# Performance work log

Measured on AMD Instinct MI355X. Metric: run time of the kernel, lower is better.

## Reference

```python
import jax, jax.numpy as jnp
import numpy as np

N_BITS = 8
Q_LEVELS = N_BITS ** 2 - 1  # note: original uses n_bits**2 - 1, not 2**n_bits - 1
GRID_RES = (128, 512, 2048)  # 2**7, 2**9, 2**11
BITWIDTH = 6
CODE_SIZE = 4


def _qround(x, axis):
    mn = jnp.min(x, axis=axis, keepdims=True)
    mx = jnp.max(x, axis=axis, keepdims=True)
    scale = jnp.maximum(mx - mn, 1e-8) / Q_LEVELS
    return jnp.round((x - mn) / scale) * scale + mn


def _ste(q, x):
    # straight-through estimator: forward q, gradient of x
    return jax.lax.stop_gradient(q - x) + x


def _qalinear(x, w, b):
    w_q = _ste(_qround(w, (-2, -1)), w)
    b_q = _ste(_qround(b, -1), b)
    return x @ w_q + b_q


def _grid(coords, indices, codebook, res):
    # coords: [N] in [-1, 1]; indices: [res, 2**bitwidth]; codebook: [2**bitwidth, code_size]
    soft_grid = jax.nn.softmax(indices, axis=-1) @ codebook           # [res, C]
    max_grid = codebook[jnp.argmax(indices, axis=1)]                  # [res, C]
    grid = _ste(max_grid, soft_grid)
    c = (coords + 1.0) / 2.0 * (res - 1)
    left = jnp.minimum(jnp.floor(c), res - 2).astype(jnp.int32)
    right = jnp.maximum(jnp.ceil(c), 1).astype(jnp.int32)
    w = (c - left)[..., None]                                         # [N, 1]
    return (1.0 - w) * grid[left] + w * grid[right]                   # [N, C]


def setup_inputs() -> dict:
    key = jax.random.key(0)
    ks = jax.random.split(key, 20)
    N = 1 << 20
    x_coord = jax.random.uniform(ks[0], (N, 1), jnp.float32, -1.0, 1.0)
    x_feat = jax.random.uniform(ks[1], (N, 1), jnp.float32, -1.0, 1.0)
    x = jnp.concatenate([x_feat, x_coord], axis=-1)  # last dim is the grid coordinate
    inp = {"x": x}
    for gi, res in enumerate(GRID_RES):
        inp[f"cb{gi}"] = 0.01 * jax.random.normal(ks[2 + 2 * gi], (2 ** BITWIDTH, CODE_SIZE), jnp.float32)
        inp[f"ind{gi}"] = 0.01 * jax.random.normal(ks[3 + 2 * gi], (res, 2 ** BITWIDTH), jnp.float32)
    dims = [(5, 64), (64, 64), (64, 64), (64, 64), (64, 1)]
    for li, (di, do) in enumerate(dims):
        inp[f"w{li}"] = (2 * jax.random.uniform(ks[8 + 2 * li], (di, do), jnp.float32) - 1) / np.sqrt(di)
        inp[f"b{li}"] = (2 * jax.random.uniform(ks[9 + 2 * li], (do,), jnp.float32) - 1) / np.sqrt(di)
    return inp


def reference(x, cb0, ind0, cb1, ind1, cb2, ind2,
              w0, b0, w1, b1, w2, b2, w3, b3, w4, b4):
    coords = x[..., -1]
    g = (_grid(coords, ind0, cb0, GRID_RES[0])
         + _grid(coords, ind1, cb1, GRID_RES[1])
         + _grid(coords, ind2, cb2, GRID_RES[2]))           # [N, 4]
    h = jnp.concatenate([g, x[..., :-1]], axis=-1)          # [N, 5]
    h = _qalinear(h, w0, b0)
    for w, b in ((w1, b1), (w2, b2), (w3, b3)):
        h = _qalinear(jax.nn.gelu(h, approximate=False), w, b)
    h = _qalinear(jax.nn.gelu(h, approximate=False), w4, b4)
    return jnp.tanh(h)
```

## Files before the change

kernel.cpp:

```cpp
#include <hip/hip_runtime.h>
#include <hip/hip_bf16.h>
#include <math.h>

#define WQ0 0
#define BQ0 320
#define WQ1 384
#define BQ1 4480
#define WQ2 4544
#define BQ2 8640
#define WQ3 8704
#define BQ3 12800
#define WQ4 12864
#define BQ4 12928
#define GT0 12932
#define GT1 13444
#define GT2 15492
#define FRAG_OFF 23684
#define NFRAG 28
#define W4P 38020
#define WSCALE 64.0f
#define WINV   0.015625f

typedef _Float16 f16x8 __attribute__((ext_vector_type(8)));
typedef _Float16 f16x2 __attribute__((ext_vector_type(2)));
typedef float floatx4 __attribute__((ext_vector_type(4)));
typedef float floatx2 __attribute__((ext_vector_type(2)));
typedef unsigned int uintx4 __attribute__((ext_vector_type(4)));

__device__ inline floatx4 mfma16(f16x8 a, f16x8 b, floatx4 c) {
    return __builtin_amdgcn_mfma_f32_16x16x32_f16(a, b, c, 0, 0, 0);
}
__device__ inline floatx2 splat2(float c) { return (floatx2){c, c}; }

__device__ inline unsigned int pkrtz(float a, float b) {
    auto r = __builtin_amdgcn_cvt_pkrtz(a, b);
    return __builtin_bit_cast(unsigned int, r);
}
__device__ inline unsigned int pack_f16(float a, float b) {
    unsigned short ua = __builtin_bit_cast(unsigned short, (_Float16)a);
    unsigned short ub = __builtin_bit_cast(unsigned short, (_Float16)b);
    return (unsigned int)ua | ((unsigned int)ub << 16);
}
__device__ inline f16x8 frag_from(uint2 a, uint2 b) {
    uintx4 u = {a.x, a.y, b.x, b.y};
    return __builtin_bit_cast(f16x8, u);
}
__device__ inline f16x2 h2(unsigned int u) { return __builtin_bit_cast(f16x2, u); }

#if __has_builtin(__builtin_amdgcn_fdot2)
__device__ inline float fdot2f(f16x2 a, f16x2 b, float c) {
    return __builtin_amdgcn_fdot2(a, b, c, false);
}
#else
__device__ inline float fdot2f(f16x2 a, f16x2 b, float c) {
    return fmaf((float)a[0], (float)b[0], fmaf((float)a[1], (float)b[1], c));
}
#endif

__device__ inline floatx2 gelu2(floatx2 x) {
    floatx2 ax = __builtin_elementwise_abs(x);
    floatx2 z  = ax * splat2(0.70710678118654752f);
    floatx2 den = __builtin_elementwise_fma(z, splat2(0.47047f), splat2(1.0f));
    floatx2 t;
    t.x = __builtin_amdgcn_rcpf(den.x);
    t.y = __builtin_amdgcn_rcpf(den.y);
    floatx2 p = __builtin_elementwise_fma(t, splat2(0.7478556f), splat2(-0.0958798f));
    p = __builtin_elementwise_fma(t, p, splat2(0.3480242f));
    p = p * t;
    floatx2 ea = (z * z) * splat2(-1.44269504088896f);
    floatx2 e;
    e.x = __builtin_amdgcn_exp2f(ea.x);
    e.y = __builtin_amdgcn_exp2f(ea.y);
    floatx2 er = __builtin_elementwise_fma(-p, e, splat2(1.0f));
    return __builtin_elementwise_fma(ax, er, x) * splat2(0.5f);
}

__device__ inline float tanh_fast(float x) {
    float e = __builtin_amdgcn_exp2f(x * 2.88539008177793f);
    return fmaf(-2.0f, __builtin_amdgcn_rcpf(e + 1.0f), 1.0f);
}

__device__ void block_minmax(float mn, float mx, float* omn, float* omx,
                             float* smn, float* smx) {
    __syncthreads();
    #pragma unroll
    for (int off = 32; off > 0; off >>= 1) {
        mn = fminf(mn, __shfl_down(mn, off));
        mx = fmaxf(mx, __shfl_down(mx, off));
    }
    int wid = threadIdx.x >> 6, lane = threadIdx.x & 63;
    if (lane == 0) { smn[wid] = mn; smx[wid] = mx; }
    __syncthreads();
    if (threadIdx.x == 0) {
        float a = smn[0], b = smx[0];
        for (int i = 1; i < 4; ++i) { a = fminf(a, smn[i]); b = fmaxf(b, smx[i]); }
        smn[0] = a; smx[0] = b;
    }
    __syncthreads();
    *omn = smn[0]; *omx = smx[0];
}

__device__ void quantize_tensor(const float* __restrict__ src, int n,
                                float* __restrict__ dst, float* smn, float* smx) {
    float mn = 3.4e38f, mx = -3.4e38f;
    for (int i = threadIdx.x; i < n; i += blockDim.x) {
        float v = src[i];
        mn = fminf(mn, v); mx = fmaxf(mx, v);
    }
    float gmn, gmx;
    block_minmax(mn, mx, &gmn, &gmx, smn, smx);
    float scale = fmaxf(gmx - gmn, 1e-8f) / 63.0f;
    for (int i = threadIdx.x; i < n; i += blockDim.x) {
        float v = src[i];
        dst[i] = rintf((v - gmn) / scale) * scale + gmn;
    }
}

__global__ void vinr_prep(
    const float* __restrict__ cb0, const float* __restrict__ ind0,
    const float* __restrict__ cb1, const float* __restrict__ ind1,
    const float* __restrict__ cb2, const float* __restrict__ ind2,
    const float* __restrict__ w0, const float* __restrict__ b0,
    const float* __restrict__ w1, const float* __restrict__ b1,
    const float* __restrict__ w2, const float* __restrict__ b2,
    const float* __restrict__ w3, const float* __restrict__ b3,
    const float* __restrict__ w4, const float* __restrict__ b4,
    float* __restrict__ ws)
{
    __shared__ float smn[4], smx[4];
    if (blockIdx.x < 10) {
        switch (blockIdx.x) {
            case 0: quantize_tensor(w0, 320, ws + WQ0, smn, smx); break;
            case 1: quantize_tensor(b0, 64, ws + BQ0, smn, smx); break;
            case 2: quantize_tensor(w1, 4096, ws + WQ1, smn, smx); break;
            case 3: quantize_tensor(b1, 64, ws + BQ1, smn, smx); break;
            case 4: quantize_tensor(w2, 4096, ws + WQ2, smn, smx); break;
            case 5: quantize_tensor(b2, 64, ws + BQ2, smn, smx); break;
            case 6: quantize_tensor(w3, 4096, ws + WQ3, smn, smx); break;
            case 7: quantize_tensor(b3, 64, ws + BQ3, smn, smx); break;
            case 8: quantize_tensor(w4, 64, ws + WQ4, smn, smx); break;
            case 9: quantize_tensor(b4, 1, ws + BQ4, smn, smx); break;
        }
    } else if (blockIdx.x < 21) {
        int r = (int)(blockIdx.x - 10) * 256 + (int)threadIdx.x;
        const float* ind = nullptr; const float* cb = nullptr; float* dst = nullptr;
        if (r < 128)       { ind = ind0 + r * 64;          cb = cb0; dst = ws + GT0 + r * 4; }
        else if (r < 640)  { int rr = r - 128;  ind = ind1 + rr * 64; cb = cb1; dst = ws + GT1 + rr * 4; }
        else if (r < 2688) { int rr = r - 640;  ind = ind2 + rr * 64; cb = cb2; dst = ws + GT2 + rr * 4; }
        if (dst) {
            float best = -3.4e38f; int bi = 0;
            for (int j = 0; j < 64; ++j) {
                float v = ind[j];
                if (v > best) { best = v; bi = j; }
            }
            #pragma unroll
            for (int d = 0; d < 4; ++d) dst[d] = cb[bi * 4 + d];
        }
    } else if (blockIdx.x < 45) {
        if (threadIdx.x < 64) {
            int fi = (int)blockIdx.x - 21;
            int lane = (int)threadIdx.x;
            int l = fi >> 3, s = (fi >> 2) & 1, ft = fi & 3;
            const float* w = (l == 0) ? w1 : (l == 1) ? w2 : w3;
            float mn = 3.4e38f, mx = -3.4e38f;
            for (int i = lane; i < 4096; i += 64) {
                float v = w[i];
                mn = fminf(mn, v); mx = fmaxf(mx, v);
            }
            #pragma unroll
            for (int off = 32; off > 0; off >>= 1) {
                mn = fminf(mn, __shfl_xor(mn, off));
                mx = fmaxf(mx, __shfl_xor(mx, off));
            }
            float scale = fmaxf(mx - mn, 1e-8f) / 63.0f;
            int q = lane >> 4, m15 = lane & 15;
            int n = ft * 16 + m15;
            f16x8 hi;
            #pragma unroll
            for (int j = 0; j < 8; ++j) {
                int k = s * 32 + q * 8 + j;
                float v = w[k * 64 + n];
                v = (rintf((v - mn) / scale) * scale + mn) * WSCALE;
                hi[j] = (_Float16)v;
            }
            f16x8* base = (f16x8*)(ws + FRAG_OFF);
            base[fi * 64 + lane] = hi;
        }
    } else if (blockIdx.x == 45) {
        int wv = (int)threadIdx.x >> 6;
        int lane = (int)threadIdx.x & 63;
        if (wv < 4) {
            float mn = 3.4e38f, mx = -3.4e38f;
            for (int i = lane; i < 320; i += 64) {
                float v = w0[i];
                mn = fminf(mn, v); mx = fmaxf(mx, v);
            }
            #pragma unroll
            for (int off = 32; off > 0; off >>= 1) {
                mn = fminf(mn, __shfl_xor(mn, off));
                mx = fmaxf(mx, __shfl_xor(mx, off));
            }
            float scale = fmaxf(mx - mn, 1e-8f) / 63.0f;
            int q = lane >> 4, m15 = lane & 15;
            int n = wv * 16 + m15;
            f16x8 hi;
            #pragma unroll
            for (int j = 0; j < 8; ++j) {
                int k = q * 8 + j;
                float v = 0.0f;
                if (k < 5) {
                    float vv = w0[k * 64 + n];
                    v = (rintf((vv - mn) / scale) * scale + mn) * WSCALE;
                }
                hi[j] = (_Float16)v;
            }
            f16x8* base = (f16x8*)(ws + FRAG_OFF);
            base[(24 + wv) * 64 + lane] = hi;
        }
    } else {
        if (threadIdx.x < 64) {
            int lane = (int)threadIdx.x;
            float v = w4[lane];
            float mn = v, mx = v;
            #pragma unroll
            for (int off = 32; off > 0; off >>= 1) {
                mn = fminf(mn, __shfl_xor(mn, off));
                mx = fmaxf(mx, __shfl_xor(mx, off));
            }
            float scale = fmaxf(mx - mn, 1e-8f) / 63.0f;
            if (lane < 32) {
                float q0 = (rintf((w4[2 * lane] - mn) / scale) * scale + mn) * WSCALE;
                float q1 = (rintf((w4[2 * lane + 1] - mn) / scale) * scale + mn) * WSCALE;
                unsigned int* wsU = (unsigned int*)ws;
                wsU[W4P + lane] = pack_f16(q0, q1);
            }
        }
    }
}

#define PSTR 38

__global__ __launch_bounds__(256, 4) void vinr_main(
    const float* __restrict__ x, const float* __restrict__ ws,
    float* __restrict__ out, int N)
{
    __shared__ __align__(16) unsigned int hlds[4 * 32 * PSTR];
    int wave = threadIdx.x >> 6, lane = threadIdx.x & 63;
    int q = lane >> 4, m15 = lane & 15;
    int p = lane & 31, half = lane >> 5;
    unsigned int* slice = hlds + wave * (32 * PSTR);

    int idx = (int)blockIdx.x * 128 + wave * 32 + p;
    int idxc = min(idx, N - 1);
    float2 xr = ((const float2*)x)[idxc];
    float feat  = xr.x;
    float coord = xr.y;

    float g0 = 0.f, g1 = 0.f, g2 = 0.f, g3 = 0.f;
    const int RES[3]  = {128, 512, 2048};
    const int GOFF[3] = {GT0, GT1, GT2};
    #pragma unroll
    for (int gi = 0; gi < 3; ++gi) {
        int res = RES[gi];
        float c = (coord + 1.0f) * 0.5f * (float)(res - 1);
        int left  = min((int)floorf(c), res - 2);
        int right = max((int)ceilf(c), 1);
        float w = c - (float)left;
        const float4* gt = (const float4*)(ws + GOFF[gi]);
        float4 gl = gt[left];
        float4 gr = gt[right];
        float wm = 1.0f - w;
        g0 += wm * gl.x + w * gr.x;
        g1 += wm * gl.y + w * gr.y;
        g2 += wm * gl.z + w * gr.z;
        g3 += wm * gl.w + w * gr.w;
    }

    const f16x8* fh = (const f16x8*)(ws + FRAG_OFF);
    f16x8 zfrag = __builtin_bit_cast(f16x8, (uintx4){0u, 0u, 0u, 0u});

    if (half == 0) {
        unsigned int* row = slice + p * PSTR;
        *(uint2*)row       = make_uint2(pack_f16(g0, g1), pack_f16(g2, g3));
        *(uint2*)(row + 2) = make_uint2(pack_f16(feat, 0.0f), 0u);
    }

    {
        f16x8 Wh[4];
        #pragma unroll
        for (int ft = 0; ft < 4; ++ft)
            Wh[ft] = fh[(24 + ft) * 64 + lane];
        f16x8 B[2];
        #pragma unroll
        for (int pt = 0; pt < 2; ++pt) {
            B[pt] = zfrag;
            if (q == 0) {
                const unsigned int* rp = slice + (pt * 16 + m15) * PSTR;
                B[pt] = frag_from(*(const uint2*)rp, *(const uint2*)(rp + 2));
            }
        }
        floatx4 acc[4][2];
        #pragma unroll
        for (int ft = 0; ft < 4; ++ft)
            #pragma unroll
            for (int pt = 0; pt < 2; ++pt)
                acc[ft][pt] = (floatx4){0.f, 0.f, 0.f, 0.f};
        #pragma unroll
        for (int ft = 0; ft < 4; ++ft)
            #pragma unroll
            for (int pt = 0; pt < 2; ++pt)
                acc[ft][pt] = mfma16(Wh[ft], B[pt], acc[ft][pt]);
        #pragma unroll
        for (int ft = 0; ft < 4; ++ft) {
            float4 b4 = *(const float4*)(ws + BQ0 + ft * 16 + q * 4);
            #pragma unroll
            for (int pt = 0; pt < 2; ++pt) {
                floatx4 av = acc[ft][pt];
                floatx2 a01 = __builtin_elementwise_fma((floatx2){av[0], av[1]},
                                  splat2(WINV), (floatx2){b4.x, b4.y});
                floatx2 a23 = __builtin_elementwise_fma((floatx2){av[2], av[3]},
                                  splat2(WINV), (floatx2){b4.z, b4.w});
                floatx2 v01 = gelu2(a01);
                floatx2 v23 = gelu2(a23);
                *(uint2*)(slice + (pt * 16 + m15) * PSTR + 8 * ft + 2 * q) =
                    make_uint2(pkrtz(v01.x, v01.y), pkrtz(v23.x, v23.y));
            }
        }
    }

    const int BQL[3] = {BQ1, BQ2, BQ3};
    #pragma unroll
    for (int l = 0; l < 3; ++l) {
        floatx4 acc[4][2];
        #pragma unroll
        for (int ft = 0; ft < 4; ++ft)
            #pragma unroll
            for (int pt = 0; pt < 2; ++pt)
                acc[ft][pt] = (floatx4){0.f, 0.f, 0.f, 0.f};

        #pragma unroll
        for (int s = 0; s < 2; ++s) {
            f16x8 Wh[4];
            #pragma unroll
            for (int ft = 0; ft < 4; ++ft)
                Wh[ft] = fh[((l * 2 + s) * 4 + ft) * 64 + lane];
            f16x8 B[2];
            #pragma unroll
            for (int pt = 0; pt < 2; ++pt) {
                const unsigned int* rp =
                    slice + (pt * 16 + m15) * PSTR + 16 * s + 4 * q;
                B[pt] = frag_from(*(const uint2*)rp, *(const uint2*)(rp + 2));
            }
            #pragma unroll
            for (int ft = 0; ft < 4; ++ft)
                #pragma unroll
                for (int pt = 0; pt < 2; ++pt)
                    acc[ft][pt] = mfma16(Wh[ft], B[pt], acc[ft][pt]);
        }
        #pragma unroll
        for (int ft = 0; ft < 4; ++ft) {
            float4 b4 = *(const float4*)(ws + BQL[l] + ft * 16 + q * 4);
            #pragma unroll
            for (int pt = 0; pt < 2; ++pt) {
                floatx4 av = acc[ft][pt];
                floatx2 a01 = __builtin_elementwise_fma((floatx2){av[0], av[1]},
                                  splat2(WINV), (floatx2){b4.x, b4.y});
                floatx2 a23 = __builtin_elementwise_fma((floatx2){av[2], av[3]},
                                  splat2(WINV), (floatx2){b4.z, b4.w});
                floatx2 v01 = gelu2(a01);
                floatx2 v23 = gelu2(a23);
                *(uint2*)(slice + (pt * 16 + m15) * PSTR + 8 * ft + 2 * q) =
                    make_uint2(pkrtz(v01.x, v01.y), pkrtz(v23.x, v23.y));
            }
        }
    }

    {
        const unsigned int* wsU = (const unsigned int*)ws;
        const unsigned int* base = slice + p * PSTR + 16 * half;
        int wb = W4P + 16 * half;
        float ah = 0.0f;
        #pragma unroll
        for (int c = 0; c < 8; ++c) {
            uint2 r = *(const uint2*)(base + 2 * c);
            ah = fdot2f(h2(r.x), h2(wsU[wb + 2 * c]),     ah);
            ah = fdot2f(h2(r.y), h2(wsU[wb + 2 * c + 1]), ah);
        }
        float acc4 = fmaf(ah, WINV, (half == 0) ? ws[BQ4] : 0.0f);
        acc4 += __shfl_xor(acc4, 32);
        if (half == 0 && idx < N) out[idx] = tanh_fast(acc4);
    }
}

extern "C" void kernel_launch(void* const* d_in, const int* in_sizes, int n_in,
                              void* d_out, int out_size, void* d_ws, size_t ws_size,
                              hipStream_t stream) {
    const float* x    = (const float*)d_in[0];
    const float* cb0  = (const float*)d_in[1];
    const float* ind0 = (const float*)d_in[2];
    const float* cb1  = (const float*)d_in[3];
    const float* ind1 = (const float*)d_in[4];
    const float* cb2  = (const float*)d_in[5];
    const float* ind2 = (const float*)d_in[6];
    const float* w0 = (const float*)d_in[7],  * b0 = (const float*)d_in[8];
    const float* w1 = (const float*)d_in[9],  * b1 = (const float*)d_in[10];
    const float* w2 = (const float*)d_in[11], * b2 = (const float*)d_in[12];
    const float* w3 = (const float*)d_in[13], * b3 = (const float*)d_in[14];
    const float* w4 = (const float*)d_in[15], * b4 = (const float*)d_in[16];
    float* ws  = (float*)d_ws;
    float* out = (float*)d_out;

    int N = in_sizes[0] / 2;

    vinr_prep<<<47, 256, 0, stream>>>(cb0, ind0, cb1, ind1, cb2, ind2,
                                      w0, b0, w1, b1, w2, b2, w3, b3, w4, b4, ws);
    int blocks = (N + 127) / 128;
    vinr_main<<<blocks, 256, 0, stream>>>(x, ws, out, N);
}
```

Baseline: 214.4 us.

## Keep MLP activations in registers by permuting weight fragment K-order

```diff
diff --git a/kernel.cpp b/kernel.cpp
--- a/kernel.cpp
+++ b/kernel.cpp
@@ -2,21 +2,15 @@
 #include <hip/hip_bf16.h>
 #include <math.h>
 
-#define WQ0 0
 #define BQ0 320
-#define WQ1 384
 #define BQ1 4480
-#define WQ2 4544
 #define BQ2 8640
-#define WQ3 8704
 #define BQ3 12800
-#define WQ4 12864
 #define BQ4 12928
 #define GT0 12932
 #define GT1 13444
 #define GT2 15492
 #define FRAG_OFF 23684
-#define NFRAG 28
 #define W4P 38020
 #define WSCALE 64.0f
 #define WINV   0.015625f
@@ -128,21 +122,16 @@
     float* __restrict__ ws)
 {
     __shared__ float smn[4], smx[4];
-    if (blockIdx.x < 10) {
+    if (blockIdx.x < 5) {
         switch (blockIdx.x) {
-            case 0: quantize_tensor(w0, 320, ws + WQ0, smn, smx); break;
-            case 1: quantize_tensor(b0, 64, ws + BQ0, smn, smx); break;
-            case 2: quantize_tensor(w1, 4096, ws + WQ1, smn, smx); break;
-            case 3: quantize_tensor(b1, 64, ws + BQ1, smn, smx); break;
-            case 4: quantize_tensor(w2, 4096, ws + WQ2, smn, smx); break;
-            case 5: quantize_tensor(b2, 64, ws + BQ2, smn, smx); break;
-            case 6: quantize_tensor(w3, 4096, ws + WQ3, smn, smx); break;
-            case 7: quantize_tensor(b3, 64, ws + BQ3, smn, smx); break;
-            case 8: quantize_tensor(w4, 64, ws + WQ4, smn, smx); break;
-            case 9: quantize_tensor(b4, 1, ws + BQ4, smn, smx); break;
-        }
-    } else if (blockIdx.x < 21) {
-        int r = (int)(blockIdx.x - 10) * 256 + (int)threadIdx.x;
+            case 0: quantize_tensor(b0, 64, ws + BQ0, smn, smx); break;
+            case 1: quantize_tensor(b1, 64, ws + BQ1, smn, smx); break;
+            case 2: quantize_tensor(b2, 64, ws + BQ2, smn, smx); break;
+            case 3: quantize_tensor(b3, 64, ws + BQ3, smn, smx); break;
+            case 4: quantize_tensor(b4, 1,  ws + BQ4, smn, smx); break;
+        }
+    } else if (blockIdx.x < 16) {
+        int r = (int)(blockIdx.x - 5) * 256 + (int)threadIdx.x;
         const float* ind = nullptr; const float* cb = nullptr; float* dst = nullptr;
         if (r < 128)       { ind = ind0 + r * 64;          cb = cb0; dst = ws + GT0 + r * 4; }
         else if (r < 640)  { int rr = r - 128;  ind = ind1 + rr * 64; cb = cb1; dst = ws + GT1 + rr * 4; }
@@ -156,9 +145,9 @@
             #pragma unroll
             for (int d = 0; d < 4; ++d) dst[d] = cb[bi * 4 + d];
         }
-    } else if (blockIdx.x < 45) {
+    } else if (blockIdx.x < 40) {
         if (threadIdx.x < 64) {
-            int fi = (int)blockIdx.x - 21;
+            int fi = (int)blockIdx.x - 16;
             int lane = (int)threadIdx.x;
             int l = fi >> 3, s = (fi >> 2) & 1, ft = fi & 3;
             const float* w = (l == 0) ? w1 : (l == 1) ? w2 : w3;
@@ -178,7 +167,7 @@
             f16x8 hi;
             #pragma unroll
             for (int j = 0; j < 8; ++j) {
-                int k = s * 32 + q * 8 + j;
+                int k = s * 32 + (j >> 2) * 16 + q * 4 + (j & 3);
                 float v = w[k * 64 + n];
                 v = (rintf((v - mn) / scale) * scale + mn) * WSCALE;
                 hi[j] = (_Float16)v;
@@ -186,7 +175,7 @@
             f16x8* base = (f16x8*)(ws + FRAG_OFF);
             base[fi * 64 + lane] = hi;
         }
-    } else if (blockIdx.x == 45) {
+    } else if (blockIdx.x == 40) {
         int wv = (int)threadIdx.x >> 6;
         int lane = (int)threadIdx.x & 63;
         if (wv < 4) {
@@ -229,28 +218,31 @@
             }
             float scale = fmaxf(mx - mn, 1e-8f) / 63.0f;
             if (lane < 32) {
-                float q0 = (rintf((w4[2 * lane] - mn) / scale) * scale + mn) * WSCALE;
-                float q1 = (rintf((w4[2 * lane + 1] - mn) / scale) * scale + mn) * WSCALE;
+                int t0 = 2 * lane, t1 = t0 + 1;
+                int f0 = ((t0 >> 5) * 32) + (((t0 >> 2) & 1) * 16)
+                       + (((t0 >> 3) & 3) * 4) + (t0 & 3);
+                int f1 = ((t1 >> 5) * 32) + (((t1 >> 2) & 1) * 16)
+                       + (((t1 >> 3) & 3) * 4) + (t1 & 3);
+                float q0 = (rintf((w4[f0] - mn) / scale) * scale + mn) * WSCALE;
+                float q1 = (rintf((w4[f1] - mn) / scale) * scale + mn) * WSCALE;
                 unsigned int* wsU = (unsigned int*)ws;
                 wsU[W4P + lane] = pack_f16(q0, q1);
             }
         }
     }
 }
-
-#define PSTR 38
 
 __global__ __launch_bounds__(256, 4) void vinr_main(
     const float* __restrict__ x, const float* __restrict__ ws,
     float* __restrict__ out, int N)
 {
-    __shared__ __align__(16) unsigned int hlds[4 * 32 * PSTR];
+    __shared__ __align__(16) uint4 ilds[4][32];
     int wave = threadIdx.x >> 6, lane = threadIdx.x & 63;
     int q = lane >> 4, m15 = lane & 15;
     int p = lane & 31, half = lane >> 5;
-    unsigned int* slice = hlds + wave * (32 * PSTR);
-
-    int idx = (int)blockIdx.x * 128 + wave * 32 + p;
+
+    int base = (int)blockIdx.x * 128 + wave * 32;
+    int idx = base + p;
     int idxc = min(idx, N - 1);
     float2 xr = ((const float2*)x)[idxc];
     float feat  = xr.x;
@@ -276,119 +268,106 @@
         g3 += wm * gl.w + w * gr.w;
     }
 
+    if (half == 0)
+        ilds[wave][p] = make_uint4(pack_f16(g0, g1), pack_f16(g2, g3),
+                                   pack_f16(feat, 0.0f), 0u);
+
     const f16x8* fh = (const f16x8*)(ws + FRAG_OFF);
     f16x8 zfrag = __builtin_bit_cast(f16x8, (uintx4){0u, 0u, 0u, 0u});
 
-    if (half == 0) {
-        unsigned int* row = slice + p * PSTR;
-        *(uint2*)row       = make_uint2(pack_f16(g0, g1), pack_f16(g2, g3));
-        *(uint2*)(row + 2) = make_uint2(pack_f16(feat, 0.0f), 0u);
-    }
-
-    {
-        f16x8 Wh[4];
+    f16x8 Bc[2][2];
+    floatx4 acc[4][2];
+    const int BOFF[4] = {BQ0, BQ1, BQ2, BQ3};
+
+    #pragma unroll
+    for (int l = 0; l < 4; ++l) {
         #pragma unroll
         for (int ft = 0; ft < 4; ++ft)
-            Wh[ft] = fh[(24 + ft) * 64 + lane];
-        f16x8 B[2];
-        #pragma unroll
-        for (int pt = 0; pt < 2; ++pt) {
-            B[pt] = zfrag;
-            if (q == 0) {
-                const unsigned int* rp = slice + (pt * 16 + m15) * PSTR;
-                B[pt] = frag_from(*(const uint2*)rp, *(const uint2*)(rp + 2));
-            }
-        }
-        floatx4 acc[4][2];
-        #pragma unroll
-        for (int ft = 0; ft < 4; ++ft)
             #pragma unroll
             for (int pt = 0; pt < 2; ++pt)
                 acc[ft][pt] = (floatx4){0.f, 0.f, 0.f, 0.f};
+
+        if (l == 0) {
+            f16x8 B0[2];
+            #pragma unroll
+            for (int pt = 0; pt < 2; ++pt) {
+                B0[pt] = zfrag;
+                if (q == 0) {
+                    uint4 r = ilds[wave][pt * 16 + m15];
+                    B0[pt] = frag_from(make_uint2(r.x, r.y), make_uint2(r.z, r.w));
+                }
+            }
+            #pragma unroll
+            for (int ft = 0; ft < 4; ++ft) {
+                f16x8 Wh = fh[(24 + ft) * 64 + lane];
+                #pragma unroll
+                for (int pt = 0; pt < 2; ++pt)
+                    acc[ft][pt] = mfma16(Wh, B0[pt], acc[ft][pt]);
+            }
+        } else {
+            #pragma unroll
+            for (int s = 0; s < 2; ++s) {
+                #pragma unroll
+                for (int ft = 0; ft < 4; ++ft) {
+                    f16x8 Wh = fh[(((l - 1) * 2 + s) * 4 + ft) * 64 + lane];
+                    #pragma unroll
+                    for (int pt = 0; pt < 2; ++pt)
+                        acc[ft][pt] = mfma16(Wh, Bc[s][pt], acc[ft][pt]);
+                }
+            }
+        }
+
+        int bb = BOFF[l];
         #pragma unroll
-        for (int ft = 0; ft < 4; ++ft)
-            #pragma unroll
-            for (int pt = 0; pt < 2; ++pt)
-                acc[ft][pt] = mfma16(Wh[ft], B[pt], acc[ft][pt]);
-        #pragma unroll
-        for (int ft = 0; ft < 4; ++ft) {
-            float4 b4 = *(const float4*)(ws + BQ0 + ft * 16 + q * 4);
+        for (int sh = 0; sh < 2; ++sh) {
+            float4 bA = *(const float4*)(ws + bb + (2 * sh)     * 16 + q * 4);
+            float4 bB = *(const float4*)(ws + bb + (2 * sh + 1) * 16 + q * 4);
             #pragma unroll
             for (int pt = 0; pt < 2; ++pt) {
-                floatx4 av = acc[ft][pt];
-                floatx2 a01 = __builtin_elementwise_fma((floatx2){av[0], av[1]},
-                                  splat2(WINV), (floatx2){b4.x, b4.y});
-                floatx2 a23 = __builtin_elementwise_fma((floatx2){av[2], av[3]},
-                                  splat2(WINV), (floatx2){b4.z, b4.w});
-                floatx2 v01 = gelu2(a01);
-                floatx2 v23 = gelu2(a23);
-                *(uint2*)(slice + (pt * 16 + m15) * PSTR + 8 * ft + 2 * q) =
-                    make_uint2(pkrtz(v01.x, v01.y), pkrtz(v23.x, v23.y));
-            }
-        }
-    }
-
-    const int BQL[3] = {BQ1, BQ2, BQ3};
-    #pragma unroll
-    for (int l = 0; l < 3; ++l) {
-        floatx4 acc[4][2];
-        #pragma unroll
-        for (int ft = 0; ft < 4; ++ft)
-            #pragma unroll
-            for (int pt = 0; pt < 2; ++pt)
-                acc[ft][pt] = (floatx4){0.f, 0.f, 0.f, 0.f};
-
+                floatx4 a0 = acc[2 * sh][pt];
+                floatx4 a1 = acc[2 * sh + 1][pt];
+                floatx2 u01 = gelu2(__builtin_elementwise_fma(
+                    (floatx2){a0[0], a0[1]}, splat2(WINV), (floatx2){bA.x, bA.y}));
+                floatx2 u23 = gelu2(__builtin_elementwise_fma(
+                    (floatx2){a0[2], a0[3]}, splat2(WINV), (floatx2){bA.z, bA.w}));
+                floatx2 v01 = gelu2(__builtin_elementwise_fma(
+                    (floatx2){a1[0], a1[1]}, splat2(WINV), (floatx2){bB.x, bB.y}));
+                floatx2 v23 = gelu2(__builtin_elementwise_fma(
+                    (floatx2){a1[2], a1[3]}, splat2(WINV), (floatx2){bB.z, bB.w}));
+                uintx4 wv = {pkrtz(u01.x, u01.y), pkrtz(u23.x, u23.y),
+                             pkrtz(v01.x, v01.y), pkrtz(v23.x, v23.y)};
+                Bc[sh][pt] = __builtin_bit_cast(f16x8, wv);
+            }
+        }
+    }
+
+    {
+        const unsigned int* wsU = (const unsigned int*)ws;
+        float ah0 = 0.0f, ah1 = 0.0f;
         #pragma unroll
         for (int s = 0; s < 2; ++s) {
-            f16x8 Wh[4];
-            #pragma unroll
-            for (int ft = 0; ft < 4; ++ft)
-                Wh[ft] = fh[((l * 2 + s) * 4 + ft) * 64 + lane];
-            f16x8 B[2];
-            #pragma unroll
-            for (int pt = 0; pt < 2; ++pt) {
-                const unsigned int* rp =
-                    slice + (pt * 16 + m15) * PSTR + 16 * s + 4 * q;
-                B[pt] = frag_from(*(const uint2*)rp, *(const uint2*)(rp + 2));
-            }
-            #pragma unroll
-            for (int ft = 0; ft < 4; ++ft)
-                #pragma unroll
-                for (int pt = 0; pt < 2; ++pt)
-                    acc[ft][pt] = mfma16(Wh[ft], B[pt], acc[ft][pt]);
-        }
-        #pragma unroll
-        for (int ft = 0; ft < 4; ++ft) {
-            float4 b4 = *(const float4*)(ws + BQL[l] + ft * 16 + q * 4);
-            #pragma unroll
-            for (int pt = 0; pt < 2; ++pt) {
-                floatx4 av = acc[ft][pt];
-                floatx2 a01 = __builtin_elementwise_fma((floatx2){av[0], av[1]},
-                                  splat2(WINV), (floatx2){b4.x, b4.y});
-                floatx2 a23 = __builtin_elementwise_fma((floatx2){av[2], av[3]},
-                                  splat2(WINV), (floatx2){b4.z, b4.w});
-                floatx2 v01 = gelu2(a01);
-                floatx2 v23 = gelu2(a23);
-                *(uint2*)(slice + (pt * 16 + m15) * PSTR + 8 * ft + 2 * q) =
-                    make_uint2(pkrtz(v01.x, v01.y), pkrtz(v23.x, v23.y));
-            }
-        }
-    }
-
-    {
-        const unsigned int* wsU = (const unsigned int*)ws;
-        const unsigned int* base = slice + p * PSTR + 16 * half;
-        int wb = W4P + 16 * half;
-        float ah = 0.0f;
-        #pragma unroll
-        for (int c = 0; c < 8; ++c) {
-            uint2 r = *(const uint2*)(base + 2 * c);
-            ah = fdot2f(h2(r.x), h2(wsU[wb + 2 * c]),     ah);
-            ah = fdot2f(h2(r.y), h2(wsU[wb + 2 * c + 1]), ah);
-        }
-        float acc4 = fmaf(ah, WINV, (half == 0) ? ws[BQ4] : 0.0f);
-        acc4 += __shfl_xor(acc4, 32);
-        if (half == 0 && idx < N) out[idx] = tanh_fast(acc4);
+            uint4 wv = *(const uint4*)(wsU + W4P + 16 * s + 4 * q);
+            uintx4 b0 = __builtin_bit_cast(uintx4, Bc[s][0]);
+            uintx4 b1 = __builtin_bit_cast(uintx4, Bc[s][1]);
+            ah0 = fdot2f(h2(b0[0]), h2(wv.x), ah0);
+            ah1 = fdot2f(h2(b1[0]), h2(wv.x), ah1);
+            ah0 = fdot2f(h2(b0[1]), h2(wv.y), ah0);
+            ah1 = fdot2f(h2(b1[1]), h2(wv.y), ah1);
+            ah0 = fdot2f(h2(b0[2]), h2(wv.z), ah0);
+            ah1 = fdot2f(h2(b1[2]), h2(wv.z), ah1);
+            ah0 = fdot2f(h2(b0[3]), h2(wv.w), ah0);
+            ah1 = fdot2f(h2(b1[3]), h2(wv.w), ah1);
+        }
+        ah0 += __shfl_xor(ah0, 16);
+        ah0 += __shfl_xor(ah0, 32);
+        ah1 += __shfl_xor(ah1, 16);
+        ah1 += __shfl_xor(ah1, 32);
+        float b4v = ws[BQ4];
+        int oidx = base + lane;
+        if (lane < 32 && oidx < N) {
+            float sel = (lane & 16) ? ah1 : ah0;
+            out[oidx] = tanh_fast(fmaf(sel, WINV, b4v));
+        }
     }
 }
 
@@ -412,7 +391,7 @@
 
     int N = in_sizes[0] / 2;
 
-    vinr_prep<<<47, 256, 0, stream>>>(cb0, ind0, cb1, ind1, cb2, ind2,
+    vinr_prep<<<42, 256, 0, stream>>>(cb0, ind0, cb1, ind1, cb2, ind2,
                                       w0, b0, w1, b1, w2, b2, w3, b3, w4, b4, ws);
     int blocks = (N + 127) / 128;
     vinr_main<<<blocks, 256, 0, stream>>>(x, ws, out, N);
```

After: 211.4 us. About the same (-1.4%).
